# Optimization experiments

Measured on AMD Instinct MI355X. Metric: run time of the kernel, lower is better.

The kernel has to match this reference:

```python
import math
import jax, jax.numpy as jnp
import numpy as np

DIM = 4096
N_HEADS = 32
N_KV_HEADS = 8
HEAD_DIM = DIM // N_HEADS        # 128
N_REP = N_HEADS // N_KV_HEADS    # 4
BSZ = 1
SEQ = 2048
ROPE_THETA = 500000.0


def setup_inputs() -> dict:
    key = jax.random.key(0)
    ks = jax.random.split(key, 5)
    scale = 1.0 / math.sqrt(DIM)
    x = jax.random.normal(ks[0], (BSZ, SEQ, DIM), dtype=jnp.float32)
    wq = jax.random.normal(ks[1], (N_HEADS * HEAD_DIM, DIM), dtype=jnp.float32) * scale
    wk = jax.random.normal(ks[2], (N_KV_HEADS * HEAD_DIM, DIM), dtype=jnp.float32) * scale
    wv = jax.random.normal(ks[3], (N_KV_HEADS * HEAD_DIM, DIM), dtype=jnp.float32) * scale
    wo = jax.random.normal(ks[4], (N_HEADS * HEAD_DIM, DIM), dtype=jnp.float32).T * scale
    wo = jnp.asarray(wo)  # [DIM, N_HEADS*HEAD_DIM] like nn.Linear(in=heads*hd, out=dim).weight
    # RoPE tables: freqs_cis[t, j] = exp(i * t * theta^{-2j/head_dim}), j in [0, head_dim/2)
    inv_freq = 1.0 / (ROPE_THETA ** (np.arange(0, HEAD_DIM, 2, dtype=np.float32) / HEAD_DIM))
    t = np.arange(SEQ, dtype=np.float32)
    ang = np.outer(t, inv_freq)  # [SEQ, HEAD_DIM//2]
    freqs_cos = jnp.asarray(np.cos(ang), dtype=jnp.float32)
    freqs_sin = jnp.asarray(np.sin(ang), dtype=jnp.float32)
    # additive causal mask [SEQ, SEQ]
    mask = jnp.where(jnp.tril(jnp.ones((SEQ, SEQ), dtype=bool)), 0.0, -1e9).astype(jnp.float32)
    return {"x": x, "wq": wq, "wk": wk, "wv": wv, "wo": wo,
            "freqs_cos": freqs_cos, "freqs_sin": freqs_sin, "mask": mask}


def _apply_rope(xh, cos, sin):
    # xh: [b, s, h, head_dim]; cos/sin: [s, head_dim//2]
    b, s, h, d = xh.shape
    xr = xh.reshape(b, s, h, d // 2, 2)
    x0, x1 = xr[..., 0], xr[..., 1]
    c = cos[None, :, None, :]
    sn = sin[None, :, None, :]
    o0 = x0 * c - x1 * sn
    o1 = x0 * sn + x1 * c
    return jnp.stack([o0, o1], axis=-1).reshape(b, s, h, d)


def reference(x, wq, wk, wv, wo, freqs_cos, freqs_sin, mask):
    bsz, seqlen, _ = x.shape
    xq = (x @ wq.T).reshape(bsz, seqlen, N_HEADS, HEAD_DIM)
    xk = (x @ wk.T).reshape(bsz, seqlen, N_KV_HEADS, HEAD_DIM)
    xv = (x @ wv.T).reshape(bsz, seqlen, N_KV_HEADS, HEAD_DIM)
    xq = _apply_rope(xq, freqs_cos, freqs_sin)
    xk = _apply_rope(xk, freqs_cos, freqs_sin)
    # repeat_kv (GQA expansion)
    keys = jnp.repeat(xk, N_REP, axis=2)    # [b, s, N_HEADS, hd]
    values = jnp.repeat(xv, N_REP, axis=2)
    scores = jnp.einsum('bqhd,bkhd->bhqk', xq, keys) / math.sqrt(HEAD_DIM)
    scores = scores + mask[None, None, :, :]
    scores = jax.nn.softmax(scores.astype(jnp.float32), axis=-1).astype(xq.dtype)
    out = jnp.einsum('bhqk,bkhd->bqhd', scores, values)
    out = out.reshape(bsz, seqlen, N_HEADS * HEAD_DIM)
    return out @ wo.T
```

## Files before the change

kernel.cpp:

```cpp
#include <hip/hip_runtime.h>
#include <math.h>
#include <stdint.h>
#include <stddef.h>


typedef __attribute__((ext_vector_type(8))) short bf16x8;
typedef __attribute__((ext_vector_type(4))) short bf16x4;
typedef __attribute__((ext_vector_type(4))) float f32x4;
typedef unsigned short u16;

#define NEG_BIG (-1.0e9f)
#define MFMA32(a, b, c) __builtin_amdgcn_mfma_f32_16x16x32_bf16(a, b, c, 0, 0, 0)

__device__ __forceinline__ float bf2f(u16 b) {
    return __uint_as_float(((unsigned int)b) << 16);
}
__device__ __forceinline__ u16 f2bf(float f) {
    unsigned int u = __float_as_uint(f);
    u += 0x7fff + ((u >> 16) & 1);
    return (u16)(u >> 16);
}
__device__ __forceinline__ void gld_lds16(short* lds, const u16* g) {
    __builtin_amdgcn_global_load_lds(
        (const __attribute__((address_space(1))) void*)g,
        (__attribute__((address_space(3))) void*)lds, 16, 0, 0);
}

__global__ __launch_bounds__(256) void cvt_bf16(const float* __restrict__ src,
                                                u16* __restrict__ dst, int n) {
    int i = (blockIdx.x * blockDim.x + threadIdx.x) * 8;
    if (i >= n) return;
    float4 a, b;
    __builtin_memcpy(&a, src + i, 16);
    __builtin_memcpy(&b, src + i + 4, 16);
    bf16x8 o;
    o[0] = (short)f2bf(a.x); o[1] = (short)f2bf(a.y);
    o[2] = (short)f2bf(a.z); o[3] = (short)f2bf(a.w);
    o[4] = (short)f2bf(b.x); o[5] = (short)f2bf(b.y);
    o[6] = (short)f2bf(b.z); o[7] = (short)f2bf(b.w);
    __builtin_memcpy(dst + i, &o, 16);
}


#define G8_STGA(bf_, ks_, kt_)                                               \
    {                                                                        \
        _Pragma("unroll") for (int r_ = 0; r_ < RA; ++r_)                    \
            gld_lds16(Ad + (bf_) * AT + (ks_) * AH + r_ * 4096,              \
                      Ag + gK * r_ + (size_t)(kt_) * 64 + (ks_) * 32);       \
    }
#define G8_STGB(bf_, ks_, kt_)                                               \
    {                                                                        \
        _Pragma("unroll") for (int r_ = 0; r_ < RB; ++r_)                    \
            gld_lds16(Bd + (bf_) * BT + (ks_) * BH + r_ * 4096,              \
                      Bg + gK * r_ + (size_t)(kt_) * 64 + (ks_) * 32);       \
    }
#define G8_PHASE(bf_, ks_, mh_, RDB_, STAGE_, WAIT_)                         \
    {                                                                        \
        if (RDB_) {                                                          \
            _Pragma("unroll") for (int n_ = 0; n_ < 4; ++n_)                 \
                __builtin_memcpy(&bfr[n_], Bs + (bf_) * BT + (ks_) * BH +    \
                                               bbase + n_ * 512, 16);        \
        }                                                                    \
        _Pragma("unroll") for (int i_ = 0; i_ < 4; ++i_)                     \
            __builtin_memcpy(&af[i_], S + (bf_) * AT + (ks_) * AH + abase +  \
                                          ((mh_) * 64 + i_ * 16) * 32, 16);  \
        STAGE_;                                                              \
        __builtin_amdgcn_s_barrier();                                        \
        asm volatile("s_waitcnt lgkmcnt(0)" ::: "memory");                   \
        __builtin_amdgcn_s_setprio(1);                                       \
        _Pragma("unroll") for (int i_ = 0; i_ < 4; ++i_)                     \
            _Pragma("unroll") for (int n_ = 0; n_ < 4; ++n_)                 \
                acc[(mh_) * 4 + i_][n_] =                                    \
                    MFMA32(af[i_], bfr[n_], acc[(mh_) * 4 + i_][n_]);        \
        __builtin_amdgcn_s_setprio(0);                                       \
        WAIT_;                                                               \
        __builtin_amdgcn_s_barrier();                                        \
    }

template <int BM, int BN, int MH, int OUT>
__device__ __forceinline__ void gemm8p(const u16* __restrict__ A,
                                       const u16* __restrict__ B,
                                       void* __restrict__ C,
                                       int mb, int nb, int N, int K,
                                       short* __restrict__ S) {
    constexpr int AT = BM * 64, BT = BN * 64;
    constexpr int AH = BM * 32, BH = BN * 32;
    constexpr int RA = BM / 128, RB = BN / 128;
    short* const Bs = S + 2 * AT;

    const int t = threadIdx.x;
    const int lane = t & 63, l15 = lane & 15, quad = lane >> 4;
    const int wid = t >> 6, wr = wid >> 2, wc = wid & 3;

    const int srow = t >> 2;
    const int cs = (t & 3) ^ ((t >> 3) & 3);
    const u16* const Ag = A + (size_t)(mb * BM + srow) * K + cs * 8;
    const u16* const Bg = B + (size_t)(nb * BN + srow) * K + cs * 8;
    short* const Ad = S + t * 8;
    short* const Bd = Bs + t * 8;
    const size_t gK = (size_t)128 * K;

    const int swz = (quad ^ ((l15 >> 1) & 3)) * 8;
    const int abase = (wr * (BM / 2) + l15) * 32 + swz;
    const int bbase = (wc * 64 + l15) * 32 + swz;

    f32x4 acc[MH * 4][4] = {};
    bf16x8 af[4], bfr[4];

    G8_STGA(0, 0, 0); G8_STGB(0, 0, 0);
    G8_STGA(0, 1, 0); G8_STGB(0, 1, 0);
    G8_STGA(1, 0, 1); G8_STGB(1, 0, 1);
    if constexpr (MH == 2) {
        asm volatile("s_waitcnt vmcnt(4)" ::: "memory");
    } else {
        asm volatile("s_waitcnt vmcnt(6)" ::: "memory");
    }
    __builtin_amdgcn_s_barrier();

    const int nIt = K >> 7;
    if constexpr (MH == 2) {
        for (int it = 0; it < nIt; ++it) {
            const int k0 = 2 * it, k1 = k0 + 1;
            const bool nl = (it < nIt - 1);
            G8_PHASE(0, 0, 0, true,  G8_STGA(1, 1, k1), );
            G8_PHASE(0, 0, 1, false, G8_STGB(1, 1, k1), );
            G8_PHASE(0, 1, 0, true,  if (nl) G8_STGA(0, 0, k0 + 2), );
            G8_PHASE(0, 1, 1, false, if (nl) G8_STGB(0, 0, k0 + 2),
                     if (nl) { asm volatile("s_waitcnt vmcnt(4)" ::: "memory"); }
                     else    { asm volatile("s_waitcnt vmcnt(0)" ::: "memory"); });
            G8_PHASE(1, 0, 0, true,  if (nl) G8_STGA(0, 1, k0 + 2), );
            G8_PHASE(1, 0, 1, false, if (nl) G8_STGB(0, 1, k0 + 2), );
            G8_PHASE(1, 1, 0, true,  if (nl) G8_STGA(1, 0, k1 + 2), );
            G8_PHASE(1, 1, 1, false, if (nl) G8_STGB(1, 0, k1 + 2),
                     if (nl) { asm volatile("s_waitcnt vmcnt(4)" ::: "memory"); });
        }
    } else {
        for (int it = 0; it < nIt - 1; ++it) {
            const int k0 = 2 * it, k1 = k0 + 1;
            G8_PHASE(0, 0, 0, true, { G8_STGA(1, 1, k1); G8_STGB(1, 1, k1); },
                     asm volatile("s_waitcnt vmcnt(6)" ::: "memory"));
            G8_PHASE(0, 1, 0, true, { G8_STGA(0, 0, k0 + 2); G8_STGB(0, 0, k0 + 2); },
                     asm volatile("s_waitcnt vmcnt(6)" ::: "memory"));
            G8_PHASE(1, 0, 0, true, { G8_STGA(0, 1, k0 + 2); G8_STGB(0, 1, k0 + 2); },
                     asm volatile("s_waitcnt vmcnt(6)" ::: "memory"));
            G8_PHASE(1, 1, 0, true, { G8_STGA(1, 0, k1 + 2); G8_STGB(1, 0, k1 + 2); },
                     asm volatile("s_waitcnt vmcnt(6)" ::: "memory"));
        }
        {
            const int k1 = (K >> 6) - 1;
            G8_PHASE(0, 0, 0, true, { G8_STGA(1, 1, k1); G8_STGB(1, 1, k1); },
                     asm volatile("s_waitcnt vmcnt(6)" ::: "memory"));
            G8_PHASE(0, 1, 0, true, ,
                     asm volatile("s_waitcnt vmcnt(3)" ::: "memory"));
            G8_PHASE(1, 0, 0, true, ,
                     asm volatile("s_waitcnt vmcnt(0)" ::: "memory"));
            G8_PHASE(1, 1, 0, true, , );
        }
    }

#pragma unroll
    for (int i8 = 0; i8 < MH * 4; ++i8) {
        const int rowb = mb * BM + wr * (BM / 2) + (i8 >> 2) * 64 +
                         (i8 & 3) * 16 + quad * 4;
#pragma unroll
        for (int j = 0; j < 4; ++j) {
            const int col = nb * BN + wc * 64 + j * 16 + l15;
            if (OUT == 2) {
                bf16x4 v;
#pragma unroll
                for (int r = 0; r < 4; ++r) v[r] = (short)f2bf(acc[i8][j][r]);
                __builtin_memcpy((u16*)C + (size_t)col * 2048 + rowb, &v, 8);
            } else if (OUT == 1) {
#pragma unroll
                for (int r = 0; r < 4; ++r)
                    ((float*)C)[(size_t)(rowb + r) * N + col] = acc[i8][j][r];
            } else {
#pragma unroll
                for (int r = 0; r < 4; ++r)
                    ((u16*)C)[(size_t)(rowb + r) * N + col] =
                        f2bf(acc[i8][j][r]);
            }
        }
    }
}

__global__ __launch_bounds__(512, 2) void qkv_proj8(
    const u16* __restrict__ x,
    const u16* __restrict__ wq, const u16* __restrict__ wk,
    const u16* __restrict__ wv,
    u16* __restrict__ Q, u16* __restrict__ Kc, u16* __restrict__ Vt) {
    __shared__ __align__(16) short S[65536];
    const int mb = blockIdx.x, y = blockIdx.y;
    if (y < 16)
        gemm8p<256, 256, 2, 0>(x, wq, Q, mb, y, 4096, 4096, S);
    else if (y < 20)
        gemm8p<256, 256, 2, 0>(x, wk, Kc, mb, y - 16, 1024, 4096, S);
    else
        gemm8p<256, 256, 2, 2>(x, wv, Vt, mb, y - 20, 1024, 4096, S);
}

__global__ __launch_bounds__(512, 2) void oproj8(
    const u16* __restrict__ A, const u16* __restrict__ wo,
    float* __restrict__ out) {
    __shared__ __align__(16) short S[49152];
    gemm8p<128, 256, 1, 1>(A, wo, out, blockIdx.x, blockIdx.y, 4096, 4096, S);
}

__global__ void rope_kernel(u16* __restrict__ X,
                            const float* __restrict__ cosb,
                            const float* __restrict__ sinb, int nheads) {
    int idx = blockIdx.x * blockDim.x + threadIdx.x;
    int total = 2048 * nheads * 64;
    if (idx >= total) return;
    int i = idx % 64;
    int h = (idx / 64) % nheads;
    int s = idx / (64 * nheads);
    u16* p = X + (size_t)s * nheads * 128 + h * 128 + 2 * i;
    float x0 = bf2f(p[0]), x1 = bf2f(p[1]);
    float c = cosb[s * 64 + i], sn = sinb[s * 64 + i];
    p[0] = f2bf(x0 * c - x1 * sn);
    p[1] = f2bf(x0 * sn + x1 * c);
}

__device__ __forceinline__ int kswz(int row, int cs) {
    int f = (row & 3) | ((row & 8) >> 1);
    return row * 128 + ((cs ^ f) << 3);
}

template <bool MASKED>
__device__ __forceinline__ void fa_step_lds(
    const short* __restrict__ Kl, const short* __restrict__ Vl,
    int kb, int q0, int l15, int quad,
    const int (&koff)[8], const int (&voff)[8],
    const bf16x8 (&qf)[4], f32x4 (&o)[8], float& m, float& l) {
    const float scale = 0.08838834764831845f;

    bf16x8 kf[8];
#pragma unroll
    for (int i = 0; i < 8; ++i) __builtin_memcpy(&kf[i], Kl + koff[i], 16);
    f32x4 s0 = {0, 0, 0, 0}, s1 = {0, 0, 0, 0};
#pragma unroll
    for (int c = 0; c < 4; ++c) {
        s0 = MFMA32(kf[c], qf[c], s0);
        s1 = MFMA32(kf[4 + c], qf[c], s1);
    }

    bf16x8 vf[8];
#pragma unroll
    for (int n = 0; n < 8; ++n) __builtin_memcpy(&vf[n], Vl + voff[n], 16);

    float sv0[4], sv1[4];
    const int q = q0 + l15;
#pragma unroll
    for (int r = 0; r < 4; ++r) {
        sv0[r] = s0[r] * scale;
        sv1[r] = s1[r] * scale;
        if (MASKED) {
            if (kb + 8 * quad + r > q) sv0[r] = NEG_BIG;
            if (kb + 8 * quad + 4 + r > q) sv1[r] = NEG_BIG;
        }
    }

    float mx = fmaxf(fmaxf(fmaxf(sv0[0], sv0[1]), fmaxf(sv0[2], sv0[3])),
                     fmaxf(fmaxf(sv1[0], sv1[1]), fmaxf(sv1[2], sv1[3])));
    mx = fmaxf(mx, __shfl_xor(mx, 16));
    mx = fmaxf(mx, __shfl_xor(mx, 32));

    float alpha = 1.0f;
    if (!__all(mx <= m + 8.0f)) {
        float mnew = fmaxf(m, mx);
        alpha = __expf(m - mnew);
        float aO[4];
#pragma unroll
        for (int r = 0; r < 4; ++r) aO[r] = __shfl(alpha, quad * 20 + r);
#pragma unroll
        for (int n = 0; n < 8; ++n)
#pragma unroll
            for (int r = 0; r < 4; ++r) o[n][r] *= aO[r];
        m = mnew;
    }

    float p0[4], p1[4], sum = 0.f;
#pragma unroll
    for (int r = 0; r < 4; ++r) {
        p0[r] = __expf(sv0[r] - m);
        p1[r] = __expf(sv1[r] - m);
        sum += p0[r] + p1[r];
    }
    sum += __shfl_xor(sum, 16);
    sum += __shfl_xor(sum, 32);
    l = l * alpha + sum;

    bf16x8 pa;
#pragma unroll
    for (int r = 0; r < 4; ++r) {
        pa[r] = (short)f2bf(p0[r]);
        pa[4 + r] = (short)f2bf(p1[r]);
    }

#pragma unroll
    for (int n = 0; n < 8; ++n) o[n] = MFMA32(pa, vf[n], o[n]);
}

__device__ __forceinline__ void fa_task(
    const u16* __restrict__ Q, const u16* __restrict__ Kc,
    const u16* __restrict__ Vt, u16* __restrict__ O,
    short* __restrict__ Kl0, short* __restrict__ Vl0,
    int q0, int nbt, int h, int kvh, int t) {
    const int lane = t & 63;
    const int l15 = lane & 15, quad = lane >> 4;

    bf16x8 qf[4];
    const u16* qp = Q + (size_t)(q0 + l15) * 4096 + h * 128 + quad * 8;
#pragma unroll
    for (int c = 0; c < 4; ++c) __builtin_memcpy(&qf[c], qp + c * 32, 16);

    const u16* ksrc[2]; short* kdst[2];
    const u16* vsrc[2]; short* vdst[2];
#pragma unroll
    for (int r = 0; r < 2; ++r) {
        int row = (t >> 4) + 16 * r;
        int slot = t & 15;
        int f = (row & 3) | ((row & 8) >> 1);
        int cks = slot ^ f;
        ksrc[r] = Kc + (size_t)row * 1024 + kvh * 128 + cks * 8;
        kdst[r] = Kl0 + (t + 256 * r) * 8;
        int rowv = (t >> 2) + 64 * r;
        int csv = (t & 3) ^ ((t >> 3) & 3);
        vsrc[r] = Vt + (size_t)(kvh * 128 + rowv) * 2048 + csv * 8;
        vdst[r] = Vl0 + (t + 256 * r) * 8;
    }

    const int rk0 = 8 * (l15 >> 2) + (l15 & 3);
    int koff[8], voff[8];
#pragma unroll
    for (int c = 0; c < 4; ++c) {
        koff[c] = kswz(rk0, quad + c * 4);
        koff[4 + c] = kswz(rk0 + 4, quad + c * 4);
    }
    const int vswz = (quad ^ ((l15 >> 1) & 3)) * 8;
#pragma unroll
    for (int n = 0; n < 8; ++n) voff[n] = (n * 16 + l15) * 32 + vswz;

    f32x4 o[8] = {};
    float m = NEG_BIG, l = 0.f;
    const int my_nb = (q0 + 47) / 32;

    {
        gld_lds16(kdst[0], ksrc[0]);
        gld_lds16(kdst[1], ksrc[1]);
        gld_lds16(vdst[0], vsrc[0]);
        gld_lds16(vdst[1], vsrc[1]);
    }
    __syncthreads();

    for (int ib = 0; ib < nbt; ++ib) {
        if (ib + 1 < nbt) {
            int kb = (ib + 1) * 32;
            int bo = ((ib + 1) & 1) * 4096;
            gld_lds16(kdst[0] + bo, ksrc[0] + (size_t)kb * 1024);
            gld_lds16(kdst[1] + bo, ksrc[1] + (size_t)kb * 1024);
            gld_lds16(vdst[0] + bo, vsrc[0] + kb);
            gld_lds16(vdst[1] + bo, vsrc[1] + kb);
        }
        if (ib < my_nb) {
            const short* Kl = Kl0 + (ib & 1) * 4096;
            const short* Vl = Vl0 + (ib & 1) * 4096;
            if (ib == my_nb - 1)
                fa_step_lds<true>(Kl, Vl, ib * 32, q0, l15, quad, koff, voff,
                                  qf, o, m, l);
            else
                fa_step_lds<false>(Kl, Vl, ib * 32, q0, l15, quad, koff, voff,
                                   qf, o, m, l);
        }
        __syncthreads();
    }

    float inv[4];
#pragma unroll
    for (int r = 0; r < 4; ++r) inv[r] = 1.f / __shfl(l, quad * 20 + r);
#pragma unroll
    for (int n = 0; n < 8; ++n)
#pragma unroll
        for (int r = 0; r < 4; ++r) {
            int row = q0 + quad * 4 + r;
            O[(size_t)row * 4096 + h * 128 + n * 16 + l15] =
                f2bf(o[n][r] * inv[r]);
        }
}

__global__ __launch_bounds__(256) void flash_attn(
    const u16* __restrict__ Q, const u16* __restrict__ Kc,
    const u16* __restrict__ Vt, u16* __restrict__ O) {
    __shared__ __align__(16) short Kl[2 * 32 * 128];
    __shared__ __align__(16) short Vl[2 * 128 * 32];
    const int pp = blockIdx.x;
    const int h = blockIdx.y;
    const int kvh = h >> 2;
    const int t = threadIdx.x, wave = t >> 6;
    fa_task(Q, Kc, Vt, O, Kl, Vl, pp * 64 + wave * 16, 2 * pp + 2, h, kvh, t);
    const int tb = 31 - pp;
    fa_task(Q, Kc, Vt, O, Kl, Vl, tb * 64 + (3 - wave) * 16, 2 * tb + 2, h,
            kvh, t);
}

extern "C" void kernel_launch(void* const* d_in, const int* in_sizes, int n_in,
                              void* d_out, int out_size, void* d_ws,
                              size_t ws_size, hipStream_t stream) {
    const float* x  = (const float*)d_in[0];
    const float* wq = (const float*)d_in[1];
    const float* wk = (const float*)d_in[2];
    const float* wv = (const float*)d_in[3];
    const float* wo = (const float*)d_in[4];
    const float* fc = (const float*)d_in[5];
    const float* fs = (const float*)d_in[6];
    float* out = (float*)d_out;

    const int NX = 2048 * 4096;
    const int NQW = 4096 * 4096;
    const int NKW = 1024 * 4096;
    const int NKV = 2048 * 1024;

    u16* Q   = (u16*)d_ws;
    u16* Kc  = Q   + NX;
    u16* Vt  = Kc  + NKV;
    u16* Ao  = Vt  + NKV;
    u16* xb  = Ao  + NX;
    u16* wqb = xb  + NX;
    u16* wkb = wqb + NQW;
    u16* wvb = wkb + NKW;
    u16* wob = wvb + NKW;

    cvt_bf16<<<NX / (256 * 8), 256, 0, stream>>>(x, xb, NX);
    cvt_bf16<<<NQW / (256 * 8), 256, 0, stream>>>(wq, wqb, NQW);
    cvt_bf16<<<NKW / (256 * 8), 256, 0, stream>>>(wk, wkb, NKW);
    cvt_bf16<<<NKW / (256 * 8), 256, 0, stream>>>(wv, wvb, NKW);
    cvt_bf16<<<NQW / (256 * 8), 256, 0, stream>>>(wo, wob, NQW);

    qkv_proj8<<<dim3(8, 24), 512, 0, stream>>>(xb, wqb, wkb, wvb, Q, Kc, Vt);
    rope_kernel<<<(2048 * 32 * 64 + 255) / 256, 256, 0, stream>>>(Q, fc, fs, 32);
    rope_kernel<<<(2048 * 8 * 64 + 255) / 256, 256, 0, stream>>>(Kc, fc, fs, 8);
    flash_attn<<<dim3(16, 32), 256, 0, stream>>>(Q, Kc, Vt, Ao);
    oproj8<<<dim3(16, 16), 512, 0, stream>>>(Ao, wob, out);
}
```

Before: 500.2 us.

## Retile QKV GEMM to 256 blocks with 128x384 tiles, fuse conversion and RoPE launches

The QKV projection moves from a 192-block grid of 256x256 tiles to 256 blocks of 128x384 tiles. Each 384-wide tile spans Q, K and V weight chunks, and blocks are remapped so their order better fills the GPU and shares cache. The five fp32-to-bf16 conversions become one launch and the two RoPE launches become one, cutting launch overhead. The output projection also gets a swizzled block order through a specialised non-template version. The larger B tile raises register pressure, and 128-row tiles lower reuse of A.

Result: no change. 509.4 us (+1.8%).

```diff
diff --git a/kernel.cpp b/kernel.cpp
--- a/kernel.cpp
+++ b/kernel.cpp
@@ -26,198 +26,257 @@
         (__attribute__((address_space(3))) void*)lds, 16, 0, 0);
 }
 
-__global__ __launch_bounds__(256) void cvt_bf16(const float* __restrict__ src,
-                                                u16* __restrict__ dst, int n) {
-    int i = (blockIdx.x * blockDim.x + threadIdx.x) * 8;
-    if (i >= n) return;
-    float4 a, b;
-    __builtin_memcpy(&a, src + i, 16);
-    __builtin_memcpy(&b, src + i + 4, 16);
+__global__ __launch_bounds__(256) void cvt_all(
+    const float* __restrict__ x, const float* __restrict__ wq,
+    const float* __restrict__ wk, const float* __restrict__ wv,
+    const float* __restrict__ wo,
+    u16* __restrict__ xb, u16* __restrict__ wqb, u16* __restrict__ wkb,
+    u16* __restrict__ wvb, u16* __restrict__ wob) {
+    const int b = blockIdx.x;
+    const float* s; u16* d; int off;
+    if (b < 4096)       { s = x;  d = xb;  off = b; }
+    else if (b < 12288) { s = wq; d = wqb; off = b - 4096; }
+    else if (b < 14336) { s = wk; d = wkb; off = b - 12288; }
+    else if (b < 16384) { s = wv; d = wvb; off = b - 14336; }
+    else                { s = wo; d = wob; off = b - 16384; }
+    const int i = off * 2048 + threadIdx.x * 8;
+    float4 a, c;
+    __builtin_memcpy(&a, s + i, 16);
+    __builtin_memcpy(&c, s + i + 4, 16);
     bf16x8 o;
     o[0] = (short)f2bf(a.x); o[1] = (short)f2bf(a.y);
     o[2] = (short)f2bf(a.z); o[3] = (short)f2bf(a.w);
-    o[4] = (short)f2bf(b.x); o[5] = (short)f2bf(b.y);
-    o[6] = (short)f2bf(b.z); o[7] = (short)f2bf(b.w);
-    __builtin_memcpy(dst + i, &o, 16);
+    o[4] = (short)f2bf(c.x); o[5] = (short)f2bf(c.y);
+    o[6] = (short)f2bf(c.z); o[7] = (short)f2bf(c.w);
+    __builtin_memcpy(d + i, &o, 16);
+}
+
+
+#define Q4_STGA(bf_, ks_, kt_)                                               \
+    gld_lds16(Ad + (bf_) * 8192 + (ks_) * 4096,                              \
+              Ag + (size_t)(kt_) * 64 + (ks_) * 32);
+#define Q4_STGB(bf_, ks_, kt_)                                               \
+    {                                                                        \
+        _Pragma("unroll") for (int r_ = 0; r_ < 3; ++r_)                     \
+            gld_lds16(Bd + (bf_) * 24576 + (ks_) * 12288 + r_ * 4096,        \
+                      Bgr[r_] + (size_t)(kt_) * 64 + (ks_) * 32);            \
+    }
+#define Q4_STG(bf_, ks_, kt_) { Q4_STGA(bf_, ks_, kt_); Q4_STGB(bf_, ks_, kt_); }
+
+#define Q4_PHASE(bf_, ks_, STAGE_, WAIT_)                                    \
+    {                                                                        \
+        _Pragma("unroll") for (int n_ = 0; n_ < 6; ++n_)                     \
+            __builtin_memcpy(&bfr[n_], Bs + (bf_) * 24576 + (ks_) * 12288 +  \
+                                           bbase + n_ * 512, 16);            \
+        _Pragma("unroll") for (int i_ = 0; i_ < 4; ++i_)                     \
+            __builtin_memcpy(&af[i_], S + (bf_) * 8192 + (ks_) * 4096 +      \
+                                          abase + i_ * 512, 16);             \
+        STAGE_;                                                              \
+        __builtin_amdgcn_s_barrier();                                        \
+        asm volatile("s_waitcnt lgkmcnt(0)" ::: "memory");                   \
+        __builtin_amdgcn_s_setprio(1);                                       \
+        _Pragma("unroll") for (int i_ = 0; i_ < 4; ++i_)                     \
+            _Pragma("unroll") for (int n_ = 0; n_ < 6; ++n_)                 \
+                acc[i_][n_] = MFMA32(af[i_], bfr[n_], acc[i_][n_]);          \
+        __builtin_amdgcn_s_setprio(0);                                       \
+        WAIT_;                                                               \
+        __builtin_amdgcn_s_barrier();                                        \
+    }
+
+__global__ __launch_bounds__(512, 2) void qkv_proj4(
+    const u16* __restrict__ x,
+    const u16* __restrict__ wq, const u16* __restrict__ wk,
+    const u16* __restrict__ wv,
+    u16* __restrict__ Q, u16* __restrict__ Kc, u16* __restrict__ Vt) {
+    __shared__ __align__(16) short S[65536];
+    short* const Bs = S + 16384;
+
+    const int lid = blockIdx.x;
+    const int logical = (lid & 7) * 32 + (lid >> 3);
+    const int mb = logical & 15, nb = logical >> 4;
+
+    const int t = threadIdx.x;
+    const int lane = t & 63, l15 = lane & 15, quad = lane >> 4;
+    const int wid = t >> 6, wr = wid >> 2, wc = wid & 3;
+
+    const int srow = t >> 2;
+    const int cs = (t & 3) ^ ((t >> 3) & 3);
+    const u16* const Ag = x + (size_t)(mb * 128 + srow) * 4096 + cs * 8;
+    const u16* Bgr[3];
+#pragma unroll
+    for (int r = 0; r < 3; ++r) {
+        const int chunk = nb * 3 + r;
+        const u16* base; int lrow;
+        if (chunk < 32)      { base = wq; lrow = chunk * 128; }
+        else if (chunk < 40) { base = wk; lrow = (chunk - 32) * 128; }
+        else                 { base = wv; lrow = (chunk - 40) * 128; }
+        Bgr[r] = base + (size_t)(lrow + srow) * 4096 + cs * 8;
+    }
+    short* const Ad = S + t * 8;
+    short* const Bd = Bs + t * 8;
+
+    const int swz = (quad ^ ((l15 >> 1) & 3)) * 8;
+    const int abase = (wr * 64 + l15) * 32 + swz;
+    const int bbase = (wc * 96 + l15) * 32 + swz;
+
+    f32x4 acc[4][6] = {};
+    bf16x8 af[4], bfr[6];
+
+    Q4_STG(0, 0, 0); Q4_STG(0, 1, 0); Q4_STG(1, 0, 1);
+    asm volatile("s_waitcnt vmcnt(8)" ::: "memory");
+    __builtin_amdgcn_s_barrier();
+
+    const int nIt = 32;
+    for (int it = 0; it < nIt; ++it) {
+        const int k0 = 2 * it, k1 = k0 + 1;
+        const bool nl = (it < nIt - 1);
+        Q4_PHASE(0, 0, Q4_STG(1, 1, k1),
+                 asm volatile("s_waitcnt vmcnt(8)" ::: "memory"));
+        Q4_PHASE(0, 1, if (nl) Q4_STG(0, 0, k0 + 2),
+                 if (nl) { asm volatile("s_waitcnt vmcnt(8)" ::: "memory"); }
+                 else    { asm volatile("s_waitcnt vmcnt(4)" ::: "memory"); });
+        Q4_PHASE(1, 0, if (nl) Q4_STG(0, 1, k0 + 2),
+                 if (nl) { asm volatile("s_waitcnt vmcnt(8)" ::: "memory"); }
+                 else    { asm volatile("s_waitcnt vmcnt(0)" ::: "memory"); });
+        Q4_PHASE(1, 1, if (nl) Q4_STG(1, 0, k1 + 2),
+                 if (nl) { asm volatile("s_waitcnt vmcnt(8)" ::: "memory"); });
+    }
+
+#pragma unroll
+    for (int i = 0; i < 4; ++i) {
+        const int rowb = mb * 128 + wr * 64 + i * 16 + quad * 4;
+#pragma unroll
+        for (int j = 0; j < 6; ++j) {
+            const int colb = nb * 384 + wc * 96 + j * 16;
+            const int col = colb + l15;
+            if (colb < 4096) {
+#pragma unroll
+                for (int r = 0; r < 4; ++r)
+                    Q[(size_t)(rowb + r) * 4096 + col] = f2bf(acc[i][j][r]);
+            } else if (colb < 5120) {
+#pragma unroll
+                for (int r = 0; r < 4; ++r)
+                    Kc[(size_t)(rowb + r) * 1024 + (col - 4096)] =
+                        f2bf(acc[i][j][r]);
+            } else {
+                bf16x4 v;
+#pragma unroll
+                for (int r = 0; r < 4; ++r) v[r] = (short)f2bf(acc[i][j][r]);
+                __builtin_memcpy(Vt + (size_t)(col - 5120) * 2048 + rowb,
+                                 &v, 8);
+            }
+        }
+    }
 }
 
 
 #define G8_STGA(bf_, ks_, kt_)                                               \
-    {                                                                        \
-        _Pragma("unroll") for (int r_ = 0; r_ < RA; ++r_)                    \
-            gld_lds16(Ad + (bf_) * AT + (ks_) * AH + r_ * 4096,              \
-                      Ag + gK * r_ + (size_t)(kt_) * 64 + (ks_) * 32);       \
-    }
+    gld_lds16(Ad + (bf_) * 8192 + (ks_) * 4096,                              \
+              Ag + (size_t)(kt_) * 64 + (ks_) * 32);
 #define G8_STGB(bf_, ks_, kt_)                                               \
     {                                                                        \
-        _Pragma("unroll") for (int r_ = 0; r_ < RB; ++r_)                    \
-            gld_lds16(Bd + (bf_) * BT + (ks_) * BH + r_ * 4096,              \
+        _Pragma("unroll") for (int r_ = 0; r_ < 2; ++r_)                     \
+            gld_lds16(Bd + (bf_) * 16384 + (ks_) * 8192 + r_ * 4096,         \
                       Bg + gK * r_ + (size_t)(kt_) * 64 + (ks_) * 32);       \
     }
-#define G8_PHASE(bf_, ks_, mh_, RDB_, STAGE_, WAIT_)                         \
+#define G8_PHASE(bf_, ks_, STAGE_, WAIT_)                                    \
     {                                                                        \
-        if (RDB_) {                                                          \
-            _Pragma("unroll") for (int n_ = 0; n_ < 4; ++n_)                 \
-                __builtin_memcpy(&bfr[n_], Bs + (bf_) * BT + (ks_) * BH +    \
-                                               bbase + n_ * 512, 16);        \
-        }                                                                    \
+        _Pragma("unroll") for (int n_ = 0; n_ < 4; ++n_)                     \
+            __builtin_memcpy(&bfr[n_], Bs + (bf_) * 16384 + (ks_) * 8192 +   \
+                                           bbase + n_ * 512, 16);            \
         _Pragma("unroll") for (int i_ = 0; i_ < 4; ++i_)                     \
-            __builtin_memcpy(&af[i_], S + (bf_) * AT + (ks_) * AH + abase +  \
-                                          ((mh_) * 64 + i_ * 16) * 32, 16);  \
+            __builtin_memcpy(&af[i_], S + (bf_) * 8192 + (ks_) * 4096 +      \
+                                          abase + i_ * 512, 16);             \
         STAGE_;                                                              \
         __builtin_amdgcn_s_barrier();                                        \
         asm volatile("s_waitcnt lgkmcnt(0)" ::: "memory");                   \
         __builtin_amdgcn_s_setprio(1);                                       \
         _Pragma("unroll") for (int i_ = 0; i_ < 4; ++i_)                     \
             _Pragma("unroll") for (int n_ = 0; n_ < 4; ++n_)                 \
-                acc[(mh_) * 4 + i_][n_] =                                    \
-                    MFMA32(af[i_], bfr[n_], acc[(mh_) * 4 + i_][n_]);        \
+                acc[i_][n_] = MFMA32(af[i_], bfr[n_], acc[i_][n_]);          \
         __builtin_amdgcn_s_setprio(0);                                       \
         WAIT_;                                                               \
         __builtin_amdgcn_s_barrier();                                        \
     }
-
-template <int BM, int BN, int MH, int OUT>
-__device__ __forceinline__ void gemm8p(const u16* __restrict__ A,
-                                       const u16* __restrict__ B,
-                                       void* __restrict__ C,
-                                       int mb, int nb, int N, int K,
-                                       short* __restrict__ S) {
-    constexpr int AT = BM * 64, BT = BN * 64;
-    constexpr int AH = BM * 32, BH = BN * 32;
-    constexpr int RA = BM / 128, RB = BN / 128;
-    short* const Bs = S + 2 * AT;
-
-    const int t = threadIdx.x;
-    const int lane = t & 63, l15 = lane & 15, quad = lane >> 4;
-    const int wid = t >> 6, wr = wid >> 2, wc = wid & 3;
-
-    const int srow = t >> 2;
-    const int cs = (t & 3) ^ ((t >> 3) & 3);
-    const u16* const Ag = A + (size_t)(mb * BM + srow) * K + cs * 8;
-    const u16* const Bg = B + (size_t)(nb * BN + srow) * K + cs * 8;
-    short* const Ad = S + t * 8;
-    short* const Bd = Bs + t * 8;
-    const size_t gK = (size_t)128 * K;
-
-    const int swz = (quad ^ ((l15 >> 1) & 3)) * 8;
-    const int abase = (wr * (BM / 2) + l15) * 32 + swz;
-    const int bbase = (wc * 64 + l15) * 32 + swz;
-
-    f32x4 acc[MH * 4][4] = {};
-    bf16x8 af[4], bfr[4];
-
-    G8_STGA(0, 0, 0); G8_STGB(0, 0, 0);
-    G8_STGA(0, 1, 0); G8_STGB(0, 1, 0);
-    G8_STGA(1, 0, 1); G8_STGB(1, 0, 1);
-    if constexpr (MH == 2) {
-        asm volatile("s_waitcnt vmcnt(4)" ::: "memory");
-    } else {
-        asm volatile("s_waitcnt vmcnt(6)" ::: "memory");
-    }
-    __builtin_amdgcn_s_barrier();
-
-    const int nIt = K >> 7;
-    if constexpr (MH == 2) {
-        for (int it = 0; it < nIt; ++it) {
-            const int k0 = 2 * it, k1 = k0 + 1;
-            const bool nl = (it < nIt - 1);
-            G8_PHASE(0, 0, 0, true,  G8_STGA(1, 1, k1), );
-            G8_PHASE(0, 0, 1, false, G8_STGB(1, 1, k1), );
-            G8_PHASE(0, 1, 0, true,  if (nl) G8_STGA(0, 0, k0 + 2), );
-            G8_PHASE(0, 1, 1, false, if (nl) G8_STGB(0, 0, k0 + 2),
-                     if (nl) { asm volatile("s_waitcnt vmcnt(4)" ::: "memory"); }
-                     else    { asm volatile("s_waitcnt vmcnt(0)" ::: "memory"); });
-            G8_PHASE(1, 0, 0, true,  if (nl) G8_STGA(0, 1, k0 + 2), );
-            G8_PHASE(1, 0, 1, false, if (nl) G8_STGB(0, 1, k0 + 2), );
-            G8_PHASE(1, 1, 0, true,  if (nl) G8_STGA(1, 0, k1 + 2), );
-            G8_PHASE(1, 1, 1, false, if (nl) G8_STGB(1, 0, k1 + 2),
-                     if (nl) { asm volatile("s_waitcnt vmcnt(4)" ::: "memory"); });
-        }
-    } else {
-        for (int it = 0; it < nIt - 1; ++it) {
-            const int k0 = 2 * it, k1 = k0 + 1;
-            G8_PHASE(0, 0, 0, true, { G8_STGA(1, 1, k1); G8_STGB(1, 1, k1); },
-                     asm volatile("s_waitcnt vmcnt(6)" ::: "memory"));
-            G8_PHASE(0, 1, 0, true, { G8_STGA(0, 0, k0 + 2); G8_STGB(0, 0, k0 + 2); },
-                     asm volatile("s_waitcnt vmcnt(6)" ::: "memory"));
-            G8_PHASE(1, 0, 0, true, { G8_STGA(0, 1, k0 + 2); G8_STGB(0, 1, k0 + 2); },
-                     asm volatile("s_waitcnt vmcnt(6)" ::: "memory"));
-            G8_PHASE(1, 1, 0, true, { G8_STGA(1, 0, k1 + 2); G8_STGB(1, 0, k1 + 2); },
-                     asm volatile("s_waitcnt vmcnt(6)" ::: "memory"));
-        }
-        {
-            const int k1 = (K >> 6) - 1;
-            G8_PHASE(0, 0, 0, true, { G8_STGA(1, 1, k1); G8_STGB(1, 1, k1); },
-                     asm volatile("s_waitcnt vmcnt(6)" ::: "memory"));
-            G8_PHASE(0, 1, 0, true, ,
-                     asm volatile("s_waitcnt vmcnt(3)" ::: "memory"));
-            G8_PHASE(1, 0, 0, true, ,
-                     asm volatile("s_waitcnt vmcnt(0)" ::: "memory"));
-            G8_PHASE(1, 1, 0, true, , );
-        }
-    }
-
-#pragma unroll
-    for (int i8 = 0; i8 < MH * 4; ++i8) {
-        const int rowb = mb * BM + wr * (BM / 2) + (i8 >> 2) * 64 +
-                         (i8 & 3) * 16 + quad * 4;
-#pragma unroll
-        for (int j = 0; j < 4; ++j) {
-            const int col = nb * BN + wc * 64 + j * 16 + l15;
-            if (OUT == 2) {
-                bf16x4 v;
-#pragma unroll
-                for (int r = 0; r < 4; ++r) v[r] = (short)f2bf(acc[i8][j][r]);
-                __builtin_memcpy((u16*)C + (size_t)col * 2048 + rowb, &v, 8);
-            } else if (OUT == 1) {
-#pragma unroll
-                for (int r = 0; r < 4; ++r)
-                    ((float*)C)[(size_t)(rowb + r) * N + col] = acc[i8][j][r];
-            } else {
-#pragma unroll
-                for (int r = 0; r < 4; ++r)
-                    ((u16*)C)[(size_t)(rowb + r) * N + col] =
-                        f2bf(acc[i8][j][r]);
-            }
-        }
-    }
-}
-
-__global__ __launch_bounds__(512, 2) void qkv_proj8(
-    const u16* __restrict__ x,
-    const u16* __restrict__ wq, const u16* __restrict__ wk,
-    const u16* __restrict__ wv,
-    u16* __restrict__ Q, u16* __restrict__ Kc, u16* __restrict__ Vt) {
-    __shared__ __align__(16) short S[65536];
-    const int mb = blockIdx.x, y = blockIdx.y;
-    if (y < 16)
-        gemm8p<256, 256, 2, 0>(x, wq, Q, mb, y, 4096, 4096, S);
-    else if (y < 20)
-        gemm8p<256, 256, 2, 0>(x, wk, Kc, mb, y - 16, 1024, 4096, S);
-    else
-        gemm8p<256, 256, 2, 2>(x, wv, Vt, mb, y - 20, 1024, 4096, S);
-}
 
 __global__ __launch_bounds__(512, 2) void oproj8(
     const u16* __restrict__ A, const u16* __restrict__ wo,
     float* __restrict__ out) {
     __shared__ __align__(16) short S[49152];
-    gemm8p<128, 256, 1, 1>(A, wo, out, blockIdx.x, blockIdx.y, 4096, 4096, S);
-}
-
-__global__ void rope_kernel(u16* __restrict__ X,
-                            const float* __restrict__ cosb,
-                            const float* __restrict__ sinb, int nheads) {
-    int idx = blockIdx.x * blockDim.x + threadIdx.x;
-    int total = 2048 * nheads * 64;
-    if (idx >= total) return;
-    int i = idx % 64;
-    int h = (idx / 64) % nheads;
-    int s = idx / (64 * nheads);
-    u16* p = X + (size_t)s * nheads * 128 + h * 128 + 2 * i;
-    float x0 = bf2f(p[0]), x1 = bf2f(p[1]);
-    float c = cosb[s * 64 + i], sn = sinb[s * 64 + i];
+    short* const Bs = S + 16384;
+
+    const int lid = blockIdx.x;
+    const int logical = (lid & 7) * 32 + (lid >> 3);
+    const int mb = logical & 15, nb = logical >> 4;
+
+    const int t = threadIdx.x;
+    const int lane = t & 63, l15 = lane & 15, quad = lane >> 4;
+    const int wid = t >> 6, wr = wid >> 2, wc = wid & 3;
+
+    const int srow = t >> 2;
+    const int cs = (t & 3) ^ ((t >> 3) & 3);
+    const u16* const Ag = A + (size_t)(mb * 128 + srow) * 4096 + cs * 8;
+    const u16* const Bg = wo + (size_t)(nb * 256 + srow) * 4096 + cs * 8;
+    short* const Ad = S + t * 8;
+    short* const Bd = Bs + t * 8;
+    const size_t gK = (size_t)128 * 4096;
+
+    const int swz = (quad ^ ((l15 >> 1) & 3)) * 8;
+    const int abase = (wr * 64 + l15) * 32 + swz;
+    const int bbase = (wc * 64 + l15) * 32 + swz;
+
+    f32x4 acc[4][4] = {};
+    bf16x8 af[4], bfr[4];
+
+    G8_STGA(0, 0, 0); G8_STGB(0, 0, 0);
+    G8_STGA(0, 1, 0); G8_STGB(0, 1, 0);
+    G8_STGA(1, 0, 1); G8_STGB(1, 0, 1);
+    asm volatile("s_waitcnt vmcnt(6)" ::: "memory");
+    __builtin_amdgcn_s_barrier();
+
+    const int nIt = 32;
+    for (int it = 0; it < nIt; ++it) {
+        const int k0 = 2 * it, k1 = k0 + 1;
+        const bool nl = (it < nIt - 1);
+        G8_PHASE(0, 0, { G8_STGA(1, 1, k1); G8_STGB(1, 1, k1); },
+                 asm volatile("s_waitcnt vmcnt(6)" ::: "memory"));
+        G8_PHASE(0, 1, if (nl) { G8_STGA(0, 0, k0 + 2); G8_STGB(0, 0, k0 + 2); },
+                 if (nl) { asm volatile("s_waitcnt vmcnt(6)" ::: "memory"); }
+                 else    { asm volatile("s_waitcnt vmcnt(3)" ::: "memory"); });
+        G8_PHASE(1, 0, if (nl) { G8_STGA(0, 1, k0 + 2); G8_STGB(0, 1, k0 + 2); },
+                 if (nl) { asm volatile("s_waitcnt vmcnt(6)" ::: "memory"); }
+                 else    { asm volatile("s_waitcnt vmcnt(0)" ::: "memory"); });
+        G8_PHASE(1, 1, if (nl) { G8_STGA(1, 0, k1 + 2); G8_STGB(1, 0, k1 + 2); },
+                 if (nl) { asm volatile("s_waitcnt vmcnt(6)" ::: "memory"); });
+    }
+
+#pragma unroll
+    for (int i = 0; i < 4; ++i) {
+        const int rowb = mb * 128 + wr * 64 + i * 16 + quad * 4;
+#pragma unroll
+        for (int j = 0; j < 4; ++j) {
+            const int col = nb * 256 + wc * 64 + j * 16 + l15;
+#pragma unroll
+            for (int r = 0; r < 4; ++r)
+                out[(size_t)(rowb + r) * 4096 + col] = acc[i][j][r];
+        }
+    }
+}
+
+__global__ __launch_bounds__(256) void rope_all(
+    u16* __restrict__ Q, u16* __restrict__ Kc,
+    const float* __restrict__ cosb, const float* __restrict__ sinb) {
+    const int idx = blockIdx.x * blockDim.x + threadIdx.x;
+    const int i = idx & 63;
+    const int hh = (idx >> 6) % 40;
+    const int s = (idx >> 6) / 40;
+    u16* p;
+    if (hh < 32)
+        p = Q + (size_t)s * 4096 + hh * 128 + 2 * i;
+    else
+        p = Kc + (size_t)s * 1024 + (hh - 32) * 128 + 2 * i;
+    const float x0 = bf2f(p[0]), x1 = bf2f(p[1]);
+    const float c = cosb[s * 64 + i], sn = sinb[s * 64 + i];
     p[0] = f2bf(x0 * c - x1 * sn);
     p[1] = f2bf(x0 * sn + x1 * c);
 }
@@ -431,15 +490,10 @@
     u16* wvb = wkb + NKW;
     u16* wob = wvb + NKW;
 
-    cvt_bf16<<<NX / (256 * 8), 256, 0, stream>>>(x, xb, NX);
-    cvt_bf16<<<NQW / (256 * 8), 256, 0, stream>>>(wq, wqb, NQW);
-    cvt_bf16<<<NKW / (256 * 8), 256, 0, stream>>>(wk, wkb, NKW);
-    cvt_bf16<<<NKW / (256 * 8), 256, 0, stream>>>(wv, wvb, NKW);
-    cvt_bf16<<<NQW / (256 * 8), 256, 0, stream>>>(wo, wob, NQW);
-
-    qkv_proj8<<<dim3(8, 24), 512, 0, stream>>>(xb, wqb, wkb, wvb, Q, Kc, Vt);
-    rope_kernel<<<(2048 * 32 * 64 + 255) / 256, 256, 0, stream>>>(Q, fc, fs, 32);
-    rope_kernel<<<(2048 * 8 * 64 + 255) / 256, 256, 0, stream>>>(Kc, fc, fs, 8);
+    cvt_all<<<24576, 256, 0, stream>>>(x, wq, wk, wv, wo,
+                                       xb, wqb, wkb, wvb, wob);
+    qkv_proj4<<<256, 512, 0, stream>>>(xb, wqb, wkb, wvb, Q, Kc, Vt);
+    rope_all<<<20480, 256, 0, stream>>>(Q, Kc, fc, fs);
     flash_attn<<<dim3(16, 32), 256, 0, stream>>>(Q, Kc, Vt, Ao);
-    oproj8<<<dim3(16, 16), 512, 0, stream>>>(Ao, wob, out);
-}
+    oproj8<<<256, 512, 0, stream>>>(Ao, wob, out);
+}
```
